# Kernel tuning notes

Hardware: AMD Instinct MI355X
Metric: run time of the kernel (lower is better)

## Reference

```python
import jax, jax.numpy as jnp
import numpy as np

N, E, F_IN, F_HID, F_OUT, B = 50000, 800000, 128, 128, 128, 64
EPS = 1e-5


def _sage_conv(x, src, dst, w_l, b_l, w_r):
    # PyG SAGEConv (mean aggr): out = lin_l(mean_{j in N(i)} x_j) + lin_r(x_i)
    msg_sum = jax.ops.segment_sum(x[src], dst, num_segments=N)          # [N, F]
    deg = jax.ops.segment_sum(jnp.ones((src.shape[0],), x.dtype), dst, num_segments=N)
    agg = msg_sum / jnp.clip(deg, 1.0)[:, None]
    return agg @ w_l + b_l + x @ w_r


def _batch_norm(x, gamma, beta):
    # PyG BatchNorm (training): biased batch stats over the node dimension
    mu = jnp.mean(x, axis=0)
    var = jnp.mean((x - mu) ** 2, axis=0)
    return (x - mu) * jax.lax.rsqrt(var + EPS) * gamma + beta


def setup_inputs() -> dict:
    key = jax.random.key(0)
    ks = jax.random.split(key, 12)
    x = jax.random.normal(ks[0], (N, F_IN), jnp.float32)
    edge_index = jax.random.randint(ks[1], (2, E), 0, N, jnp.int64 if jax.config.jax_enable_x64 else jnp.int32)
    batch = jnp.sort(jax.random.randint(ks[2], (N,), 0, B))
    s1 = 1.0 / np.sqrt(F_IN)
    s2 = 1.0 / np.sqrt(F_HID)
    return {
        "x": x, "edge_index": edge_index, "batch": batch,
        "w_l1": jax.random.uniform(ks[3], (F_IN, F_HID), jnp.float32, -s1, s1),
        "b_l1": jax.random.uniform(ks[4], (F_HID,), jnp.float32, -s1, s1),
        "w_r1": jax.random.uniform(ks[5], (F_IN, F_HID), jnp.float32, -s1, s1),
        "g1": jnp.ones((F_HID,), jnp.float32),
        "beta1": jnp.zeros((F_HID,), jnp.float32),
        "w_l2": jax.random.uniform(ks[6], (F_HID, F_OUT), jnp.float32, -s2, s2),
        "b_l2": jax.random.uniform(ks[7], (F_OUT,), jnp.float32, -s2, s2),
        "w_r2": jax.random.uniform(ks[8], (F_HID, F_OUT), jnp.float32, -s2, s2),
        "g2": jnp.ones((F_OUT,), jnp.float32),
        "beta2": jnp.zeros((F_OUT,), jnp.float32),
    }


def reference(x, edge_index, batch, w_l1, b_l1, w_r1, g1, beta1, w_l2, b_l2, w_r2, g2, beta2):
    src, dst = edge_index[0], edge_index[1]
    h = jax.nn.relu(_batch_norm(_sage_conv(x, src, dst, w_l1, b_l1, w_r1), g1, beta1))
    h = jax.nn.relu(_batch_norm(_sage_conv(h, src, dst, w_l2, b_l2, w_r2), g2, beta2))
    # global_mean_pool over graph ids
    pooled = jax.ops.segment_sum(h, batch, num_segments=B)              # [B, F_OUT]
    cnt = jax.ops.segment_sum(jnp.ones((N,), h.dtype), batch, num_segments=B)
    return pooled / jnp.clip(cnt, 1.0)[:, None]
```

## Files before the change

### kernel.cpp

```cpp
#include <hip/hip_runtime.h>
#include <hip/hip_bf16.h>
#include <stdint.h>

typedef unsigned int uint32;
typedef unsigned short ushort16;

typedef __attribute__((ext_vector_type(8))) short short8;
typedef __attribute__((ext_vector_type(4))) float f32x4;

#define N_NODES 50000
#define N_EDGES 800000
#define FD      128
#define NGRAPH  64
#define MTILES  3125
#define NBK     196
#define GB      391
#define GB2     782
#define PCH     32
#define SBK     16
#define KCH2    25

__device__ __forceinline__ float bf2f(ushort16 u){
  union { uint32 i; float f; } v; v.i = ((uint32)u) << 16; return v.f;
}
__device__ __forceinline__ float bf2f_lo(uint32 w){ union{uint32 i;float f;}v; v.i = w << 16; return v.f; }
__device__ __forceinline__ float bf2f_hi(uint32 w){ union{uint32 i;float f;}v; v.i = w & 0xffff0000u; return v.f; }
__device__ __forceinline__ ushort16 f2bf(float f){
  uint32 u = __float_as_uint(f);
  u += 0x7fffu + ((u >> 16) & 1u);
  return (ushort16)(u >> 16);
}

__device__ __forceinline__ int ld_idx(const void* p, uint32 is64, size_t i){
  return is64 ? (int)((const long long*)p)[i] : ((const int*)p)[i];
}
__device__ __forceinline__ float ld_f(const void* p, uint32 isf32, int i){
  return isf32 ? ((const float*)p)[i] : bf2f(((const ushort16*)p)[i]);
}

__device__ __forceinline__ void get_flags(const uint32* __restrict__ xw,
    const uint32* __restrict__ eiw, uint32& isf32, uint32& is64)
{
  int l = threadIdx.x & 63;
  uint32 w = xw[l];
  uint32 e8 = (w >> 7) & 0xFFu;
  bool bf_like = (e8 >= 0x70u && e8 <= 0x82u);
  unsigned long long m = __ballot(bf_like);
  isf32 = (__popcll(m) < 32) ? 1u : 0u;
  uint32 hi = (l < 8) ? eiw[2*l + 1] : 1u;
  unsigned long long z = __ballot(hi == 0u);
  is64 = ((z & 0xFFull) == 0xFFull) ? 1u : 0u;
}


__global__ __launch_bounds__(256) void pack_gseg_prep_kernel(
    const void* __restrict__ ei, const void* __restrict__ batch,
    const void* __restrict__ X,
    const void* __restrict__ WL1, const void* __restrict__ WR1,
    const void* __restrict__ WL2, const void* __restrict__ WR2,
    uint32* __restrict__ pack0, uint32* __restrict__ hist, uint32* __restrict__ gstart,
    ushort16* __restrict__ xb, short* __restrict__ wfrag)
{
  uint32 isf32, is64;
  get_flags((const uint32*)X, (const uint32*)ei, isf32, is64);
  int tid = threadIdx.x;
  if (blockIdx.x < GB){
    __shared__ uint32 h[256];
    h[tid] = 0u;
    __syncthreads();
    int base = blockIdx.x*2048;
    for (int r = 0; r < 8; ++r){
      int i = base + r*256 + tid;
      if (i < N_EDGES){
        uint32 s = (uint32)ld_idx(ei, is64, i);
        uint32 d = (uint32)ld_idx(ei, is64, (size_t)N_EDGES + i);
        pack0[i] = (d << 16) | s;
        atomicAdd(&h[d >> 8], 1u);
      }
    }
    __syncthreads();
    hist[blockIdx.x*256 + tid] = h[tid];
  } else if (blockIdx.x < GB + 196){
    int t = (blockIdx.x - GB)*256 + tid;
    if (t >= N_NODES) return;
    int b1 = ld_idx(batch, is64, t);
    int b0 = (t == 0) ? -1 : ld_idx(batch, is64, t - 1);
    for (int g = b0 + 1; g <= b1; ++g) gstart[g] = (uint32)t;
    if (t == N_NODES - 1)
      for (int g = b1 + 1; g <= NGRAPH; ++g) gstart[g] = (uint32)N_NODES;
  } else if (blockIdx.x < GB + 196 + 3125){
    if (!isf32) return;
    size_t e = ((size_t)(blockIdx.x - GB - 196)*256 + tid)*8;
    const float* p = (const float*)X + e;
    float4 u = *(const float4*)p;
    float4 v = *(const float4*)(p + 4);
    uint4 o;
    o.x = (uint32)f2bf(u.x) | ((uint32)f2bf(u.y) << 16);
    o.y = (uint32)f2bf(u.z) | ((uint32)f2bf(u.w) << 16);
    o.z = (uint32)f2bf(v.x) | ((uint32)f2bf(v.y) << 16);
    o.w = (uint32)f2bf(v.z) | ((uint32)f2bf(v.w) << 16);
    *(uint4*)(xb + e) = o;
  } else {
    int t = (blockIdx.x - GB - 196 - 3125)*256 + tid;
    int layer = t >> 15;
    int r = t & 32767;
    int k = r >> 7, n = r & 127;
    const void* w = layer ? (k < 128 ? WL2 : WR2) : (k < 128 ? WL1 : WR1);
    int kk = k & 127;
    float wv = ld_f(w, isf32, kk*128 + n);
    int off = (((k >> 5)*8 + (n >> 4))*64 + (n & 15) + 16*((kk >> 3) & 3))*8 + (kk & 7);
    wfrag[layer*32768 + off] = (short)f2bf(wv);
  }
}


__global__ __launch_bounds__(256) void scan_part_kernel(const uint32* __restrict__ hist,
    uint32* __restrict__ part)
{
  int b = threadIdx.x, p = blockIdx.x;
  int k0 = p*KCH2, k1 = (k0 + KCH2 < GB) ? k0 + KCH2 : GB;
  uint32 sum = 0;
  for (int k = k0; k < k1; ++k) sum += hist[k*256 + b];
  part[p*256 + b] = sum;
}

__global__ __launch_bounds__(256) void scan_mid_kernel(const uint32* __restrict__ part,
    uint32* __restrict__ pbase, uint32* __restrict__ bbase)
{
  __shared__ uint32 lds[256];
  int b = threadIdx.x;
  uint32 tot = 0;
#pragma unroll
  for (int p = 0; p < SBK; ++p) tot += part[p*256 + b];
  uint32 x = tot;
  lds[b] = x; __syncthreads();
  for (int o = 1; o < 256; o <<= 1){
    uint32 y = (b >= o) ? lds[b - o] : 0u;
    __syncthreads();
    x += y; lds[b] = x;
    __syncthreads();
  }
  uint32 base = x - tot;
  if (b <= NBK) bbase[b] = (b < NBK) ? base : (uint32)N_EDGES;
  uint32 run = base;
#pragma unroll
  for (int p = 0; p < SBK; ++p){
    pbase[p*256 + b] = run;
    run += part[p*256 + b];
  }
}

__global__ __launch_bounds__(256) void scan_off_kernel(const uint32* __restrict__ hist,
    const uint32* __restrict__ pbase, uint32* __restrict__ off)
{
  int b = threadIdx.x, p = blockIdx.x;
  int k0 = p*KCH2, k1 = (k0 + KCH2 < GB) ? k0 + KCH2 : GB;
  uint32 run = pbase[p*256 + b];
  for (int k = k0; k < k1; ++k){
    off[k*256 + b] = run;
    run += hist[k*256 + b];
  }
}

__global__ __launch_bounds__(256) void scatter_kernel(const uint32* __restrict__ pack0,
    const uint32* __restrict__ off, uint32* __restrict__ pack1)
{
  __shared__ uint32 cur[256];
  int tid = threadIdx.x;
  cur[tid] = off[blockIdx.x*256 + tid];
  __syncthreads();
  int base = blockIdx.x*2048;
  for (int r = 0; r < 8; ++r){
    int i = base + r*256 + tid;
    if (i < N_EDGES){
      uint32 p = pack0[i];
      uint32 pos = atomicAdd(&cur[p >> 24], 1u);
      pack1[pos] = p;
    }
  }
}

__global__ __launch_bounds__(256) void bucket_csr_kernel(const uint32* __restrict__ pack1,
    const uint32* __restrict__ bbase, uint32* __restrict__ rowstart,
    uint32* __restrict__ deg, ushort16* __restrict__ colidx)
{
  __shared__ uint32 cnt[256];
  __shared__ uint32 lds[256];
  __shared__ uint32 cur[256];
  int tid = threadIdx.x;
  int bk = blockIdx.x;
  uint32 e0 = bbase[bk], e1 = bbase[bk + 1];
  cnt[tid] = 0u;
  __syncthreads();
  for (uint32 i = e0 + tid; i < e1; i += 256)
    atomicAdd(&cnt[(pack1[i] >> 16) & 255u], 1u);
  __syncthreads();
  uint32 v = cnt[tid];
  uint32 x = v;
  lds[tid] = x; __syncthreads();
  for (int o = 1; o < 256; o <<= 1){
    uint32 y = (tid >= o) ? lds[tid - o] : 0u;
    __syncthreads();
    x += y; lds[tid] = x;
    __syncthreads();
  }
  uint32 start = e0 + x - v;
  int node = bk*256 + tid;
  if (node < N_NODES){ rowstart[node] = start; deg[node] = v; }
  cur[tid] = start;
  __syncthreads();
  for (uint32 i = e0 + tid; i < e1; i += 256){
    uint32 p = pack1[i];
    uint32 pos = atomicAdd(&cur[(p >> 16) & 255u], 1u);
    colidx[pos] = (ushort16)(p & 0xFFFFu);
  }
}


__device__ __forceinline__ void acc8(float* a, uint4 v, const float* s0, const float* h0, int APPLY){
  float f[8];
  f[0] = bf2f_lo(v.x); f[1] = bf2f_hi(v.x);
  f[2] = bf2f_lo(v.y); f[3] = bf2f_hi(v.y);
  f[4] = bf2f_lo(v.z); f[5] = bf2f_hi(v.z);
  f[6] = bf2f_lo(v.w); f[7] = bf2f_hi(v.w);
#pragma unroll
  for (int j = 0; j < 8; ++j)
    a[j] += APPLY ? fmaxf(f[j]*s0[j] + h0[j], 0.f) : f[j];
}

template<int APPLY>
__global__ __launch_bounds__(256) void agg_kernel(const ushort16* __restrict__ Xd,
    const void* __restrict__ Xraw, const void* __restrict__ eiraw,
    const uint32* __restrict__ rowstart, const uint32* __restrict__ deg,
    const ushort16* __restrict__ colidx,
    const float* __restrict__ sc, const float* __restrict__ sh,
    ushort16* __restrict__ out)
{
  uint32 isf32, is64;
  get_flags((const uint32*)Xraw, (const uint32*)eiraw, isf32, is64);
  const ushort16* X = (APPLY == 0 && !isf32) ? (const ushort16*)Xraw : Xd;
  int t = blockIdx.x*256 + threadIdx.x;
  int node = t >> 4;
  int l = t & 15;
  uint32 st = rowstart[node];
  uint32 d  = deg[node];
  float s0[8], h0[8];
#pragma unroll
  for (int j = 0; j < 8; ++j){
    s0[j] = APPLY ? sc[l*8 + j] : 0.f;
    h0[j] = APPLY ? sh[l*8 + j] : 0.f;
  }
  float a[8];
#pragma unroll
  for (int j = 0; j < 8; ++j) a[j] = 0.f;
  const ushort16* Xl = X + l*8;
  uint32 i = 0;
  for (; i < d && ((st + i) & 3u); ++i){
    uint32 c = colidx[st + i];
    acc8(a, *(const uint4*)(Xl + (size_t)c*FD), s0, h0, APPLY);
  }
  for (; i + 8 <= d; i += 8){
    uint2 cA = *(const uint2*)(colidx + st + i);
    uint2 cB = *(const uint2*)(colidx + st + i + 4);
    uint4 v0 = *(const uint4*)(Xl + (size_t)(cA.x & 0xFFFFu)*FD);
    uint4 v1 = *(const uint4*)(Xl + (size_t)(cA.x >> 16)*FD);
    uint4 v2 = *(const uint4*)(Xl + (size_t)(cA.y & 0xFFFFu)*FD);
    uint4 v3 = *(const uint4*)(Xl + (size_t)(cA.y >> 16)*FD);
    uint4 v4 = *(const uint4*)(Xl + (size_t)(cB.x & 0xFFFFu)*FD);
    uint4 v5 = *(const uint4*)(Xl + (size_t)(cB.x >> 16)*FD);
    uint4 v6 = *(const uint4*)(Xl + (size_t)(cB.y & 0xFFFFu)*FD);
    uint4 v7 = *(const uint4*)(Xl + (size_t)(cB.y >> 16)*FD);
    acc8(a, v0, s0, h0, APPLY); acc8(a, v1, s0, h0, APPLY);
    acc8(a, v2, s0, h0, APPLY); acc8(a, v3, s0, h0, APPLY);
    acc8(a, v4, s0, h0, APPLY); acc8(a, v5, s0, h0, APPLY);
    acc8(a, v6, s0, h0, APPLY); acc8(a, v7, s0, h0, APPLY);
  }
  for (; i + 4 <= d; i += 4){
    uint2 cA = *(const uint2*)(colidx + st + i);
    uint4 v0 = *(const uint4*)(Xl + (size_t)(cA.x & 0xFFFFu)*FD);
    uint4 v1 = *(const uint4*)(Xl + (size_t)(cA.x >> 16)*FD);
    uint4 v2 = *(const uint4*)(Xl + (size_t)(cA.y & 0xFFFFu)*FD);
    uint4 v3 = *(const uint4*)(Xl + (size_t)(cA.y >> 16)*FD);
    acc8(a, v0, s0, h0, APPLY); acc8(a, v1, s0, h0, APPLY);
    acc8(a, v2, s0, h0, APPLY); acc8(a, v3, s0, h0, APPLY);
  }
  for (; i < d; ++i){
    uint32 c = colidx[st + i];
    acc8(a, *(const uint4*)(Xl + (size_t)c*FD), s0, h0, APPLY);
  }
  float inv = 1.f / fmaxf((float)d, 1.f);
  uint4 o;
  o.x = (uint32)f2bf(a[0]*inv) | ((uint32)f2bf(a[1]*inv) << 16);
  o.y = (uint32)f2bf(a[2]*inv) | ((uint32)f2bf(a[3]*inv) << 16);
  o.z = (uint32)f2bf(a[4]*inv) | ((uint32)f2bf(a[5]*inv) << 16);
  o.w = (uint32)f2bf(a[6]*inv) | ((uint32)f2bf(a[7]*inv) << 16);
  *(uint4*)(out + (size_t)node*FD + l*8) = o;
}


__device__ __forceinline__ short8 affine_relu8(short8 a, const float* sc, const float* sh, int koff){
  short8 r;
#pragma unroll
  for (int j = 0; j < 8; ++j){
    float v = bf2f((ushort16)a[j]) * sc[koff + j] + sh[koff + j];
    r[j] = (short)f2bf(fmaxf(v, 0.f));
  }
  return r;
}

template<int APPLY>
__global__ __launch_bounds__(256) void gemm_bn_kernel(
    const ushort16* __restrict__ A0, const ushort16* __restrict__ A1d,
    const void* __restrict__ A1raw, const void* __restrict__ eiraw,
    const short* __restrict__ wfrag, const void* __restrict__ bias,
    const float* __restrict__ sc, const float* __restrict__ sh,
    const void* __restrict__ Xraw,
    ushort16* __restrict__ hpre, float* __restrict__ bnpart)
{
  __shared__ float red[256];
  uint32 isf32, is64;
  get_flags((const uint32*)Xraw, (const uint32*)eiraw, isf32, is64);
  const ushort16* A1 = (A1raw && !isf32) ? (const ushort16*)A1raw : A1d;
  int tid = threadIdx.x;
  red[tid] = 0.f;
  int wave = tid >> 6, lane = tid & 63, lq = lane >> 4, lm = lane & 15;
  int mt = blockIdx.x*4 + wave;
  bool valid = mt < MTILES;
  size_t m0 = (size_t)((valid ? mt : 0)*16 + lm);
  f32x4 acc[8];
#pragma unroll
  for (int i = 0; i < 8; ++i) acc[i] = (f32x4){0.f,0.f,0.f,0.f};

#pragma unroll
  for (int ks = 0; ks < 8; ++ks){
    int koff = (ks & 3)*32 + lq*8;
    const short* srcp = (const short*)(ks < 4 ? A0 : A1);
    short8 a = *(const short8*)(srcp + m0*FD + koff);
    if (APPLY && ks >= 4) a = affine_relu8(a, sc, sh, koff);
#pragma unroll
    for (int nt = 0; nt < 8; ++nt){
      short8 b = *(const short8*)&wfrag[((ks*8 + nt)*64 + lane)*8];
      acc[nt] = __builtin_amdgcn_mfma_f32_16x16x32_bf16(a, b, acc[nt], 0, 0, 0);
    }
  }

  __syncthreads();
#pragma unroll
  for (int nt = 0; nt < 8; ++nt){
    int colc = nt*16 + lm;
    float bb = ld_f(bias, isf32, colc);
    float s = 0.f, s2 = 0.f;
    if (valid){
      size_t nb = (size_t)mt*16 + lq*4;
#pragma unroll
      for (int r = 0; r < 4; ++r){
        float val = acc[nt][r] + bb;
        hpre[(nb + r)*FD + colc] = f2bf(val);
        s += val; s2 += val*val;
      }
    }
    s  += __shfl_xor(s, 16);  s  += __shfl_xor(s, 32);
    s2 += __shfl_xor(s2, 16); s2 += __shfl_xor(s2, 32);
    if (lq == 0){
      atomicAdd(&red[colc], s);
      atomicAdd(&red[128 + colc], s2);
    }
  }
  __syncthreads();
  bnpart[blockIdx.x*256 + tid] = red[tid];
}


__global__ __launch_bounds__(256) void bn_final_kernel(const float* __restrict__ bnpart,
    const void* __restrict__ gamma, const void* __restrict__ beta,
    const void* __restrict__ Xraw, const void* __restrict__ eiraw,
    float* __restrict__ scale, float* __restrict__ shift)
{
  uint32 isf32, is64;
  get_flags((const uint32*)Xraw, (const uint32*)eiraw, isf32, is64);
  int tid = threadIdx.x;
  int f = blockIdx.x*8 + (tid >> 5);
  int l = tid & 31;
  float s = 0.f, q = 0.f;
  for (int b = l; b < GB2; b += 32){
    s += bnpart[b*256 + f];
    q += bnpart[b*256 + 128 + f];
  }
#pragma unroll
  for (int m = 16; m >= 1; m >>= 1){
    s += __shfl_xor(s, m);
    q += __shfl_xor(q, m);
  }
  if (l == 0){
    const float invN = 1.0f / (float)N_NODES;
    float mu  = s * invN;
    float var = q * invN - mu*mu;
    float scv = ld_f(gamma, isf32, f) * rsqrtf(var + 1e-5f);
    scale[f] = scv;
    shift[f] = ld_f(beta, isf32, f) - mu * scv;
  }
}


__global__ __launch_bounds__(256) void pool_partial_kernel(const ushort16* __restrict__ hp,
    const float* __restrict__ scale, const float* __restrict__ shift,
    const uint32* __restrict__ gstart, float* __restrict__ pool_part)
{
  __shared__ float wred[4*16*8];
  int tid = threadIdx.x;
  int g = blockIdx.x >> 5, chunk = blockIdx.x & 31;
  int slot = tid >> 4, l = tid & 15;
  int wave = tid >> 6, lane = tid & 63;
  uint32 st = gstart[g], cnt = gstart[g+1] - st;
  uint32 per = (cnt + PCH - 1) >> 5;
  uint32 b0 = st + chunk*per;
  uint32 b1 = b0 + per;
  uint32 e1 = st + cnt;
  if (b1 > e1) b1 = e1;
  float s0[8], h0[8], a[8];
#pragma unroll
  for (int j = 0; j < 8; ++j){ s0[j] = scale[l*8 + j]; h0[j] = shift[l*8 + j]; a[j] = 0.f; }
  for (uint32 n = b0 + slot; n < b1; n += 16){
    const uint4 v = *(const uint4*)(hp + (size_t)n*FD + l*8);
    float f[8];
    f[0] = bf2f_lo(v.x); f[1] = bf2f_hi(v.x);
    f[2] = bf2f_lo(v.y); f[3] = bf2f_hi(v.y);
    f[4] = bf2f_lo(v.z); f[5] = bf2f_hi(v.z);
    f[6] = bf2f_lo(v.w); f[7] = bf2f_hi(v.w);
#pragma unroll
    for (int j = 0; j < 8; ++j) a[j] += fmaxf(f[j]*s0[j] + h0[j], 0.f);
  }
#pragma unroll
  for (int j = 0; j < 8; ++j){
    a[j] += __shfl_xor(a[j], 16);
    a[j] += __shfl_xor(a[j], 32);
  }
  if (lane < 16){
#pragma unroll
    for (int j = 0; j < 8; ++j) wred[(wave*16 + lane)*8 + j] = a[j];
  }
  __syncthreads();
  if (tid < 16){
    float r[8];
#pragma unroll
    for (int j = 0; j < 8; ++j)
      r[j] = wred[(0*16 + tid)*8 + j] + wred[(1*16 + tid)*8 + j]
           + wred[(2*16 + tid)*8 + j] + wred[(3*16 + tid)*8 + j];
    float* dst = pool_part + (size_t)blockIdx.x*FD + tid*8;
#pragma unroll
    for (int j = 0; j < 8; ++j) dst[j] = r[j];
  }
}

__global__ void pool_final_kernel(const float* __restrict__ pool_part,
    const uint32* __restrict__ gstart, const void* __restrict__ Xraw,
    const void* __restrict__ eiraw, void* __restrict__ out)
{
  uint32 isf32, is64;
  get_flags((const uint32*)Xraw, (const uint32*)eiraw, isf32, is64);
  int t = blockIdx.x*256 + threadIdx.x;
  int g = t >> 7, f = t & 127;
  float c = fmaxf((float)(gstart[g+1] - gstart[g]), 1.f);
  float v = 0.f;
#pragma unroll 8
  for (int ch = 0; ch < PCH; ++ch)
    v += pool_part[(size_t)(g*PCH + ch)*FD + f];
  v /= c;
  if (isf32) ((float*)out)[t] = v;
  else       ((ushort16*)out)[t] = f2bf(v);
}


extern "C" void kernel_launch(void* const* d_in, const int* in_sizes, int n_in,
                              void* d_out, int out_size, void* d_ws, size_t ws_size,
                              hipStream_t stream)
{
  const void* x   = d_in[0];
  const void* ei  = d_in[1];
  const void* bat = d_in[2];
  const void* wl1 = d_in[3];
  const void* bl1 = d_in[4];
  const void* wr1 = d_in[5];
  const void* g1  = d_in[6];
  const void* be1 = d_in[7];
  const void* wl2 = d_in[8];
  const void* bl2 = d_in[9];
  const void* wr2 = d_in[10];
  const void* g2  = d_in[11];
  const void* be2 = d_in[12];
  char* ws = (char*)d_ws;

  uint32* gstart  = (uint32*)(ws + 64);
  uint32* bbase   = (uint32*)(ws + 384);
  float*  scale1  = (float*) (ws + 1280);
  float*  shift1  = (float*) (ws + 1792);
  float*  scale2  = (float*) (ws + 2304);
  float*  shift2  = (float*) (ws + 2816);
  uint32* rowstart= (uint32*)(ws + 3328);
  uint32* deg     = (uint32*)(ws + 203328);
  ushort16* colidx= (ushort16*)(ws + 403328);
  uint32* part    = (uint32*)(ws + 2003328);
  uint32* pbase   = (uint32*)(ws + 2019712);
  short*  wfrag   = (short*) (ws + 2204032);
  float*  bnpart  = (float*) (ws + 2335104);
  ushort16* xb    = (ushort16*)(ws + 3135872);
  ushort16* aggb  = (ushort16*)(ws + 15935872);
  ushort16* hp1   = (ushort16*)(ws + 28735872);
  ushort16* hp2   = (ushort16*)(ws + 41535872);
  uint32* pack0   = (uint32*)(ws + 28735872);
  uint32* pack1   = (uint32*)(ws + 31935872);
  uint32* hist    = (uint32*)(ws + 35135872);
  uint32* off     = (uint32*)(ws + 35536256);
  float*  ppart   = (float*) (ws + 28735872);

  pack_gseg_prep_kernel<<<GB + 196 + 3125 + 256, 256, 0, stream>>>(
      ei, bat, x, wl1, wr1, wl2, wr2, pack0, hist, gstart, xb, wfrag);
  scan_part_kernel <<<SBK, 256, 0, stream>>>(hist, part);
  scan_mid_kernel  <<<1,   256, 0, stream>>>(part, pbase, bbase);
  scan_off_kernel  <<<SBK, 256, 0, stream>>>(hist, pbase, off);
  scatter_kernel   <<<GB,  256, 0, stream>>>(pack0, off, pack1);
  bucket_csr_kernel<<<NBK, 256, 0, stream>>>(pack1, bbase, rowstart, deg, colidx);

  agg_kernel<0>    <<<3125, 256, 0, stream>>>(xb, x, ei, rowstart, deg, colidx,
                                              nullptr, nullptr, aggb);
  gemm_bn_kernel<0><<<GB2,  256, 0, stream>>>(aggb, xb, x, ei, wfrag, bl1,
                                              nullptr, nullptr, x, hp1, bnpart);
  bn_final_kernel  <<<16,   256, 0, stream>>>(bnpart, g1, be1, x, ei, scale1, shift1);

  agg_kernel<1>    <<<3125, 256, 0, stream>>>(hp1, x, ei, rowstart, deg, colidx,
                                              scale1, shift1, aggb);
  gemm_bn_kernel<1><<<GB2,  256, 0, stream>>>(aggb, hp1, nullptr, ei, wfrag + 32768, bl2,
                                              scale1, shift1, x, hp2, bnpart);
  bn_final_kernel  <<<16,   256, 0, stream>>>(bnpart, g2, be2, x, ei, scale2, shift2);

  pool_partial_kernel<<<NGRAPH*PCH, 256, 0, stream>>>(hp2, scale2, shift2, gstart, ppart);
  pool_final_kernel  <<<32,  256, 0, stream>>>(ppart, gstart, x, ei, d_out);
}
```

Measured before the change: 269.3 us.

## Gather neighbor features in FP8 to halve aggregation traffic

Node features are re-encoded to FP8 (e4m3) copies: x is encoded during prep, and a new z8 kernel applies BN affine+ReLU to hp1 and encodes it before layer-2 aggregation. The aggregation kernel then gathers 8-byte FP8 vectors instead of 16-byte bf16 vectors per lane and decodes with hardware cvt instructions. The goal is to cut random-gather memory traffic, at the cost of an extra pass kernel and noticeably lower precision in the aggregated means, which may threaten tolerance.

```diff
diff --git a/kernel.cpp b/kernel.cpp
--- a/kernel.cpp
+++ b/kernel.cpp
@@ -7,6 +7,7 @@
 
 typedef __attribute__((ext_vector_type(8))) short short8;
 typedef __attribute__((ext_vector_type(4))) float f32x4;
+typedef __attribute__((ext_vector_type(2))) float f32x2;
 
 #define N_NODES 50000
 #define N_EDGES 800000
@@ -38,6 +39,65 @@
   return isf32 ? ((const float*)p)[i] : bf2f(((const ushort16*)p)[i]);
 }
 
+#if __has_builtin(__builtin_amdgcn_cvt_pk_f32_fp8) && __has_builtin(__builtin_amdgcn_cvt_pk_fp8_f32)
+#define HW_FP8 1
+#else
+#define HW_FP8 0
+#endif
+
+template<bool HI>
+__device__ __forceinline__ uint32 enc_pair(float f0, float f1, uint32 old){
+#if HW_FP8
+  return (uint32)__builtin_amdgcn_cvt_pk_fp8_f32(f0, f1, (int)old, HI);
+#else
+  uint32 r = old;
+  float ff[2] = {f0, f1};
+#pragma unroll
+  for (int j = 0; j < 2; ++j){
+    uint32 u = __float_as_uint(ff[j]);
+    uint32 s = (u >> 31) << 7;
+    uint32 au = u & 0x7FFFFFFFu;
+    uint32 rr = au + 0x7FFFFu + ((au >> 20) & 1u);
+    uint32 e = rr >> 23;
+    uint32 q;
+    if (e < 121u) q = s;
+    else { uint32 m8 = ((e - 120u) << 3) | ((rr >> 20) & 7u);
+           if (m8 > 0x7Eu) m8 = 0x7Eu; q = s | m8; }
+    int sh = (HI ? 16 : 0) + j*8;
+    r = (r & ~(0xFFu << sh)) | (q << sh);
+  }
+  return r;
+#endif
+}
+
+__device__ __forceinline__ uint32 enc4(float f0, float f1, float f2, float f3){
+  uint32 w = enc_pair<false>(f0, f1, 0u);
+  return enc_pair<true>(f2, f3, w);
+}
+
+__device__ __forceinline__ float dec1(uint32 b){
+  uint32 em = b & 0x7Fu;
+  float mag = (em >= 8u) ? __uint_as_float((em + 960u) << 20)
+                         : (float)em * 0.001953125f;
+  return (b & 0x80u) ? -mag : mag;
+}
+
+__device__ __forceinline__ void acc8f8(float* a, uint2 v){
+#if HW_FP8
+  f32x2 p0 = __builtin_amdgcn_cvt_pk_f32_fp8((int)v.x, false);
+  f32x2 p1 = __builtin_amdgcn_cvt_pk_f32_fp8((int)v.x, true);
+  f32x2 p2 = __builtin_amdgcn_cvt_pk_f32_fp8((int)v.y, false);
+  f32x2 p3 = __builtin_amdgcn_cvt_pk_f32_fp8((int)v.y, true);
+  a[0] += p0[0]; a[1] += p0[1]; a[2] += p1[0]; a[3] += p1[1];
+  a[4] += p2[0]; a[5] += p2[1]; a[6] += p3[0]; a[7] += p3[1];
+#else
+#pragma unroll
+  for (int j = 0; j < 4; ++j) a[j]     += dec1((v.x >> (j*8)) & 0xFFu);
+#pragma unroll
+  for (int j = 0; j < 4; ++j) a[4 + j] += dec1((v.y >> (j*8)) & 0xFFu);
+#endif
+}
+
 __device__ __forceinline__ void get_flags(const uint32* __restrict__ xw,
     const uint32* __restrict__ eiw, uint32& isf32, uint32& is64)
 {
@@ -59,7 +119,7 @@
     const void* __restrict__ WL1, const void* __restrict__ WR1,
     const void* __restrict__ WL2, const void* __restrict__ WR2,
     uint32* __restrict__ pack0, uint32* __restrict__ hist, uint32* __restrict__ gstart,
-    ushort16* __restrict__ xb, short* __restrict__ wfrag)
+    ushort16* __restrict__ xb, uint2* __restrict__ x8, short* __restrict__ wfrag)
 {
   uint32 isf32, is64;
   get_flags((const uint32*)X, (const uint32*)ei, isf32, is64);
@@ -89,17 +149,28 @@
     if (t == N_NODES - 1)
       for (int g = b1 + 1; g <= NGRAPH; ++g) gstart[g] = (uint32)N_NODES;
   } else if (blockIdx.x < GB + 196 + 3125){
-    if (!isf32) return;
     size_t e = ((size_t)(blockIdx.x - GB - 196)*256 + tid)*8;
-    const float* p = (const float*)X + e;
-    float4 u = *(const float4*)p;
-    float4 v = *(const float4*)(p + 4);
-    uint4 o;
-    o.x = (uint32)f2bf(u.x) | ((uint32)f2bf(u.y) << 16);
-    o.y = (uint32)f2bf(u.z) | ((uint32)f2bf(u.w) << 16);
-    o.z = (uint32)f2bf(v.x) | ((uint32)f2bf(v.y) << 16);
-    o.w = (uint32)f2bf(v.z) | ((uint32)f2bf(v.w) << 16);
-    *(uint4*)(xb + e) = o;
+    float f[8];
+    if (isf32){
+      const float* p = (const float*)X + e;
+      float4 u = *(const float4*)p;
+      float4 v = *(const float4*)(p + 4);
+      f[0]=u.x; f[1]=u.y; f[2]=u.z; f[3]=u.w;
+      f[4]=v.x; f[5]=v.y; f[6]=v.z; f[7]=v.w;
+      uint4 o;
+      o.x = (uint32)f2bf(f[0]) | ((uint32)f2bf(f[1]) << 16);
+      o.y = (uint32)f2bf(f[2]) | ((uint32)f2bf(f[3]) << 16);
+      o.z = (uint32)f2bf(f[4]) | ((uint32)f2bf(f[5]) << 16);
+      o.w = (uint32)f2bf(f[6]) | ((uint32)f2bf(f[7]) << 16);
+      *(uint4*)(xb + e) = o;
+    } else {
+      uint4 v = *(const uint4*)((const ushort16*)X + e);
+      f[0]=bf2f_lo(v.x); f[1]=bf2f_hi(v.x); f[2]=bf2f_lo(v.y); f[3]=bf2f_hi(v.y);
+      f[4]=bf2f_lo(v.z); f[5]=bf2f_hi(v.z); f[6]=bf2f_lo(v.w); f[7]=bf2f_hi(v.w);
+    }
+    uint32 w0 = enc4(f[0], f[1], f[2], f[3]);
+    uint32 w1 = enc4(f[4], f[5], f[6], f[7]);
+    x8[e >> 3] = (uint2){w0, w1};
   } else {
     int t = (blockIdx.x - GB - 196 - 3125)*256 + tid;
     int layer = t >> 15;
@@ -217,7 +288,13 @@
 }
 
 
-__device__ __forceinline__ void acc8(float* a, uint4 v, const float* s0, const float* h0, int APPLY){
+__global__ __launch_bounds__(256) void z8_kernel(const ushort16* __restrict__ hp,
+    const float* __restrict__ scale, const float* __restrict__ shift,
+    uint2* __restrict__ z8)
+{
+  size_t e = ((size_t)blockIdx.x*256 + threadIdx.x)*8;
+  int c = (int)(e & 127);
+  uint4 v = *(const uint4*)(hp + e);
   float f[8];
   f[0] = bf2f_lo(v.x); f[1] = bf2f_hi(v.x);
   f[2] = bf2f_lo(v.y); f[3] = bf2f_hi(v.y);
@@ -225,68 +302,56 @@
   f[6] = bf2f_lo(v.w); f[7] = bf2f_hi(v.w);
 #pragma unroll
   for (int j = 0; j < 8; ++j)
-    a[j] += APPLY ? fmaxf(f[j]*s0[j] + h0[j], 0.f) : f[j];
-}
-
-template<int APPLY>
-__global__ __launch_bounds__(256) void agg_kernel(const ushort16* __restrict__ Xd,
-    const void* __restrict__ Xraw, const void* __restrict__ eiraw,
+    f[j] = fmaxf(f[j]*scale[c + j] + shift[c + j], 0.f);
+  uint32 w0 = enc4(f[0], f[1], f[2], f[3]);
+  uint32 w1 = enc4(f[4], f[5], f[6], f[7]);
+  z8[e >> 3] = (uint2){w0, w1};
+}
+
+
+__global__ __launch_bounds__(256) void agg_kernel(const uint2* __restrict__ X8,
     const uint32* __restrict__ rowstart, const uint32* __restrict__ deg,
-    const ushort16* __restrict__ colidx,
-    const float* __restrict__ sc, const float* __restrict__ sh,
-    ushort16* __restrict__ out)
-{
-  uint32 isf32, is64;
-  get_flags((const uint32*)Xraw, (const uint32*)eiraw, isf32, is64);
-  const ushort16* X = (APPLY == 0 && !isf32) ? (const ushort16*)Xraw : Xd;
+    const ushort16* __restrict__ colidx, ushort16* __restrict__ out)
+{
   int t = blockIdx.x*256 + threadIdx.x;
   int node = t >> 4;
   int l = t & 15;
   uint32 st = rowstart[node];
   uint32 d  = deg[node];
-  float s0[8], h0[8];
-#pragma unroll
-  for (int j = 0; j < 8; ++j){
-    s0[j] = APPLY ? sc[l*8 + j] : 0.f;
-    h0[j] = APPLY ? sh[l*8 + j] : 0.f;
-  }
   float a[8];
 #pragma unroll
   for (int j = 0; j < 8; ++j) a[j] = 0.f;
-  const ushort16* Xl = X + l*8;
+  const uint2* Xl = X8 + l;
   uint32 i = 0;
   for (; i < d && ((st + i) & 3u); ++i){
     uint32 c = colidx[st + i];
-    acc8(a, *(const uint4*)(Xl + (size_t)c*FD), s0, h0, APPLY);
+    acc8f8(a, Xl[(size_t)c*16]);
   }
   for (; i + 8 <= d; i += 8){
     uint2 cA = *(const uint2*)(colidx + st + i);
     uint2 cB = *(const uint2*)(colidx + st + i + 4);
-    uint4 v0 = *(const uint4*)(Xl + (size_t)(cA.x & 0xFFFFu)*FD);
-    uint4 v1 = *(const uint4*)(Xl + (size_t)(cA.x >> 16)*FD);
-    uint4 v2 = *(const uint4*)(Xl + (size_t)(cA.y & 0xFFFFu)*FD);
-    uint4 v3 = *(const uint4*)(Xl + (size_t)(cA.y >> 16)*FD);
-    uint4 v4 = *(const uint4*)(Xl + (size_t)(cB.x & 0xFFFFu)*FD);
-    uint4 v5 = *(const uint4*)(Xl + (size_t)(cB.x >> 16)*FD);
-    uint4 v6 = *(const uint4*)(Xl + (size_t)(cB.y & 0xFFFFu)*FD);
-    uint4 v7 = *(const uint4*)(Xl + (size_t)(cB.y >> 16)*FD);
-    acc8(a, v0, s0, h0, APPLY); acc8(a, v1, s0, h0, APPLY);
-    acc8(a, v2, s0, h0, APPLY); acc8(a, v3, s0, h0, APPLY);
-    acc8(a, v4, s0, h0, APPLY); acc8(a, v5, s0, h0, APPLY);
-    acc8(a, v6, s0, h0, APPLY); acc8(a, v7, s0, h0, APPLY);
+    uint2 v0 = Xl[(size_t)(cA.x & 0xFFFFu)*16];
+    uint2 v1 = Xl[(size_t)(cA.x >> 16)*16];
+    uint2 v2 = Xl[(size_t)(cA.y & 0xFFFFu)*16];
+    uint2 v3 = Xl[(size_t)(cA.y >> 16)*16];
+    uint2 v4 = Xl[(size_t)(cB.x & 0xFFFFu)*16];
+    uint2 v5 = Xl[(size_t)(cB.x >> 16)*16];
+    uint2 v6 = Xl[(size_t)(cB.y & 0xFFFFu)*16];
+    uint2 v7 = Xl[(size_t)(cB.y >> 16)*16];
+    acc8f8(a, v0); acc8f8(a, v1); acc8f8(a, v2); acc8f8(a, v3);
+    acc8f8(a, v4); acc8f8(a, v5); acc8f8(a, v6); acc8f8(a, v7);
   }
   for (; i + 4 <= d; i += 4){
     uint2 cA = *(const uint2*)(colidx + st + i);
-    uint4 v0 = *(const uint4*)(Xl + (size_t)(cA.x & 0xFFFFu)*FD);
-    uint4 v1 = *(const uint4*)(Xl + (size_t)(cA.x >> 16)*FD);
-    uint4 v2 = *(const uint4*)(Xl + (size_t)(cA.y & 0xFFFFu)*FD);
-    uint4 v3 = *(const uint4*)(Xl + (size_t)(cA.y >> 16)*FD);
-    acc8(a, v0, s0, h0, APPLY); acc8(a, v1, s0, h0, APPLY);
-    acc8(a, v2, s0, h0, APPLY); acc8(a, v3, s0, h0, APPLY);
+    uint2 v0 = Xl[(size_t)(cA.x & 0xFFFFu)*16];
+    uint2 v1 = Xl[(size_t)(cA.x >> 16)*16];
+    uint2 v2 = Xl[(size_t)(cA.y & 0xFFFFu)*16];
+    uint2 v3 = Xl[(size_t)(cA.y >> 16)*16];
+    acc8f8(a, v0); acc8f8(a, v1); acc8f8(a, v2); acc8f8(a, v3);
   }
   for (; i < d; ++i){
     uint32 c = colidx[st + i];
-    acc8(a, *(const uint4*)(Xl + (size_t)c*FD), s0, h0, APPLY);
+    acc8f8(a, Xl[(size_t)c*16]);
   }
   float inv = 1.f / fmaxf((float)d, 1.f);
   uint4 o;
@@ -507,6 +572,8 @@
   ushort16* aggb  = (ushort16*)(ws + 15935872);
   ushort16* hp1   = (ushort16*)(ws + 28735872);
   ushort16* hp2   = (ushort16*)(ws + 41535872);
+  uint2*  x8      = (uint2*) (ws + 41535872);
+  uint2*  z8      = (uint2*) (ws + 3135872);
   uint32* pack0   = (uint32*)(ws + 28735872);
   uint32* pack1   = (uint32*)(ws + 31935872);
   uint32* hist    = (uint32*)(ws + 35135872);
@@ -514,21 +581,20 @@
   float*  ppart   = (float*) (ws + 28735872);
 
   pack_gseg_prep_kernel<<<GB + 196 + 3125 + 256, 256, 0, stream>>>(
-      ei, bat, x, wl1, wr1, wl2, wr2, pack0, hist, gstart, xb, wfrag);
+      ei, bat, x, wl1, wr1, wl2, wr2, pack0, hist, gstart, xb, x8, wfrag);
   scan_part_kernel <<<SBK, 256, 0, stream>>>(hist, part);
   scan_mid_kernel  <<<1,   256, 0, stream>>>(part, pbase, bbase);
   scan_off_kernel  <<<SBK, 256, 0, stream>>>(hist, pbase, off);
   scatter_kernel   <<<GB,  256, 0, stream>>>(pack0, off, pack1);
   bucket_csr_kernel<<<NBK, 256, 0, stream>>>(pack1, bbase, rowstart, deg, colidx);
 
-  agg_kernel<0>    <<<3125, 256, 0, stream>>>(xb, x, ei, rowstart, deg, colidx,
-                                              nullptr, nullptr, aggb);
+  agg_kernel       <<<3125, 256, 0, stream>>>(x8, rowstart, deg, colidx, aggb);
   gemm_bn_kernel<0><<<GB2,  256, 0, stream>>>(aggb, xb, x, ei, wfrag, bl1,
                                               nullptr, nullptr, x, hp1, bnpart);
   bn_final_kernel  <<<16,   256, 0, stream>>>(bnpart, g1, be1, x, ei, scale1, shift1);
 
-  agg_kernel<1>    <<<3125, 256, 0, stream>>>(hp1, x, ei, rowstart, deg, colidx,
-                                              scale1, shift1, aggb);
+  z8_kernel        <<<3125, 256, 0, stream>>>(hp1, scale1, shift1, z8);
+  agg_kernel       <<<3125, 256, 0, stream>>>(z8, rowstart, deg, colidx, aggb);
   gemm_bn_kernel<1><<<GB2,  256, 0, stream>>>(aggb, hp1, nullptr, ei, wfrag + 32768, bl2,
                                               scale1, shift1, x, hp2, bnpart);
   bn_final_kernel  <<<16,   256, 0, stream>>>(bnpart, g2, be2, x, ei, scale2, shift2);
```

Result: faster. 248.9 us (-7.6%).
